# Kernel tuning notes

Hardware: AMD Instinct MI355X
Metric: run time of the kernel (lower is better)

The kernel has to match this reference:

```python
import jax, jax.numpy as jnp
from jax import lax
import numpy as np

P1, P2, M1, M2, WIN, STEP = 7, 7, 18, 55, 37, 4


def _unfold(x, p):
    # x: [N,C,Hp,Wp] -> [N, C*p*p, Ho*Wo], torch.nn.functional.unfold ordering (C, di, dj)
    N, C, Hp, Wp = x.shape
    Ho, Wo = Hp - p + 1, Wp - p + 1
    cols = jnp.stack([x[:, :, i:i + Ho, j:j + Wo] for i in range(p) for j in range(p)], axis=2)
    return cols.reshape(N, C * p * p, Ho * Wo)


def _reflect_unfold(x, r, p):
    return _unfold(jnp.pad(x, ((0, 0), (0, 0), (r, r), (r, r)), mode='reflect'), p)


def _fold(X, p, oh, ow):
    # inverse of unfold (sum of overlapping patches), torch.nn.functional.fold
    N, n, L = X.shape
    Ho, Wo = oh - p + 1, ow - p + 1
    C = n // (p * p)
    Xr = X.reshape(N, C, p, p, Ho, Wo)
    out = jnp.zeros((N, C, oh, ow), X.dtype)
    for i in range(p):
        for j in range(p):
            out = out.at[:, :, i:i + Ho, j:j + Wo].add(Xr[:, :, i, j])
    return out


def _block_matching(x, m, p, w, s):
    # x: [N,1,H,W] -> flat patch indices [N, B*m] into the (H+w-1)x(W+w-1) unfold grid
    N, C, H, Wd = x.shape
    inc = w // 2
    xs = _reflect_unfold(x, p // 2 + inc, p).reshape(N, p * p, H + 2 * inc, Wd + 2 * inc)
    xc = xs[:, :, inc:inc + H:s, inc:inc + Wd:s]  # [N, p*p, Hs, Ws]
    Hs, Ws = xc.shape[2], xc.shape[3]
    offs = jnp.stack(jnp.meshgrid(jnp.arange(w), jnp.arange(w), indexing='ij'), axis=-1).reshape(-1, 2)
    def d_of(off):
        xo = lax.dynamic_slice(xs, (0, 0, off[0], off[1]), (N, p * p, H, Wd))[:, :, ::s, ::s]
        return jnp.sum((xo - xc) ** 2, axis=1)  # [N, Hs, Ws]
    dist = jnp.moveaxis(lax.map(d_of, offs), 0, 1)  # [N, w*w, Hs, Ws]
    dist = dist.at[:, inc * w + inc].set(-1.0)  # force self-match first
    _, idx = lax.top_k(-jnp.transpose(dist, (0, 2, 3, 1)), m)  # smallest m, sorted
    idx = jnp.transpose(idx, (0, 3, 1, 2))  # [N, m, Hs, Ws]
    ir = idx // w - inc
    ic = idx % w - inc
    rows = inc + s * jnp.arange(Hs)
    cols = inc + s * jnp.arange(Ws)
    flat = (ir + rows[None, None, :, None]) * (Wd + w - 1) + (ic + cols[None, None, None, :])
    return jnp.transpose(flat.reshape(N, m, Hs * Ws), (0, 2, 1)).reshape(N, -1)  # [N, B*m]


def _group_patches(unf, idx, m, n):
    # unf: [N, n, L], idx: [N, B*m] -> [N, B, m, n]
    N = unf.shape[0]
    g = jnp.take_along_axis(unf, idx[:, None, :], axis=2)  # [N, n, B*m]
    return jnp.transpose(g, (0, 2, 1)).reshape(N, -1, m, n)


def _denoise1(Y, sigma):
    m, n = Y.shape[2], Y.shape[3]
    YtY = jnp.einsum('abik,abjk->abij', Y, Y)
    rhs = YtY - (n * sigma ** 2) * jnp.eye(m, dtype=Y.dtype)
    theta = jnp.swapaxes(jnp.linalg.solve(YtY, rhs), -1, -2)
    Xh = theta @ Y
    wts = 1.0 / jnp.sum(theta ** 2, axis=3, keepdims=True)
    return Xh, wts


def _denoise2(Y, X, sigma):
    m, n = X.shape[2], X.shape[3]
    XtX = jnp.einsum('abik,abjk->abij', X, X)
    A = XtX + (n * sigma ** 2) * jnp.eye(m, dtype=X.dtype)
    theta = jnp.swapaxes(jnp.linalg.solve(A, XtX), -1, -2)
    Xh = theta @ Y
    wts = 1.0 / jnp.sum(theta ** 2, axis=3, keepdims=True)
    return Xh, wts


def _aggregation(Y, wts, idx, H, Wd, L, p, w):
    # Y: [N,B,m,n], wts: [N,B,m,1], idx: [N,B*m]; scatter-add into unfold grid, fold, normalize
    N, B, m, n = Y.shape
    Yw = jnp.transpose(Y * wts, (0, 3, 1, 2)).reshape(N, n, B * m)
    wflat = jnp.broadcast_to(wts.reshape(N, 1, B * m), (N, n, B * m))
    def scat(vals, ib):
        return jnp.zeros((n, L), vals.dtype).at[:, ib].add(vals)
    Xsum = jax.vmap(scat)(Yw, idx)
    div = jax.vmap(scat)(wflat, idx)
    oh, ow = H + w - 1 + p - 1, Wd + w - 1 + p - 1
    num = _fold(Xsum, p, oh, ow)
    den = _fold(div, p, oh, ow)
    r = w // 2 + p // 2
    return (num / den)[:, :, r:-r, r:-r]


def _nlridge(input_y, sigma):
    N, C, H, Wd = input_y.shape
    w, s = WIN, STEP
    # ---- step 1 ----
    p, m = P1, M1
    yb = jnp.mean(input_y, axis=1, keepdims=True)
    idx1 = _block_matching(lax.stop_gradient(yb), m, p, w, s)
    unf_y1 = _reflect_unfold(input_y, p // 2 + w // 2, p)
    Y1 = _group_patches(unf_y1, idx1, m, C * p * p)
    Xh1, w1 = _denoise1(Y1, sigma)
    den1 = _aggregation(Xh1, w1, idx1, H, Wd, unf_y1.shape[2], p, w)
    # ---- step 2 ----
    p, m = P2, M2
    xb = jnp.mean(den1, axis=1, keepdims=True)
    idx2 = _block_matching(lax.stop_gradient(xb), m, p, w, s)
    unf_y2 = _reflect_unfold(input_y, p // 2 + w // 2, p)
    unf_x2 = _reflect_unfold(den1, p // 2 + w // 2, p)
    Y2 = _group_patches(unf_y2, idx2, m, C * p * p)
    X2 = _group_patches(unf_x2, idx2, m, C * p * p)
    Xh2, w2 = _denoise2(Y2, X2, sigma)
    return _aggregation(Xh2, w2, idx2, H, Wd, unf_y2.shape[2], p, w)


def setup_inputs() -> dict:
    key = jax.random.key(0)
    k1 = jax.random.fold_in(key, 1)
    input_y = jax.random.uniform(k1, (1, 1, 256, 256), dtype=jnp.float32)
    sigma = jnp.asarray(0.1, dtype=jnp.float32)  # ~25/255 AWGN
    return {"input_y": input_y, "sigma": sigma}


def reference(input_y, sigma):
    return _nlridge(input_y, sigma)
```

## Files before the change

### kernel.cpp

```cpp
#include <hip/hip_runtime.h>
#include <math.h>
#include <float.h>

constexpr int IMG  = 256;
constexpr int PADR = 21;
constexpr int PDIM = IMG + 2*PADR;
constexpr int XDIM = PDIM - 7 + 1;
constexpr int LTOT = XDIM * XDIM;
constexpr int WSZ  = 37;
constexpr int INC  = 18;
constexpr int ST   = 4;
constexpr int GDIM = 64;
constexpr int NBLK = GDIM * GDIM;
constexpr int PS   = 7;
constexpr int PP   = 49;
constexpr int MM1  = 18;
constexpr int MM2  = 55;
constexpr int RG   = 43;
constexpr int NOFF = WSZ * WSZ;
constexpr int UCAP = (NOFF + 63) / 64;

__global__ void pad_reflect(const float* __restrict__ src, float* __restrict__ dst)
{
    int idx = blockIdx.x * 256 + threadIdx.x;
    if (idx >= PDIM * PDIM) return;
    int y = idx / PDIM, x = idx % PDIM;
    int oy = y - PADR; oy = (oy < 0) ? -oy : ((oy >= IMG) ? 2*(IMG-1) - oy : oy);
    int ox = x - PADR; ox = (ox < 0) ? -ox : ((ox >= IMG) ? 2*(IMG-1) - ox : ox);
    dst[idx] = src[oy * IMG + ox];
}

__global__ __launch_bounds__(256) void block_match(const float* __restrict__ pad,
                                                   int* __restrict__ pos, int m)
{
    __shared__ float reg[RG][RG + 1];
    __shared__ float dist[NOFF];

    const int gi = blockIdx.y, gj = blockIdx.x;
    const int tid = threadIdx.x;
    const int r0 = ST * gi, c0 = ST * gj;

    for (int t = tid; t < RG * RG; t += 256) {
        int r = t / RG, c = t % RG;
        reg[r][c] = pad[(r0 + r) * PDIM + (c0 + c)];
    }
    __syncthreads();

    float q[PP];
#pragma unroll
    for (int i = 0; i < PS; i++)
#pragma unroll
        for (int j = 0; j < PS; j++)
            q[i * PS + j] = reg[INC + i][INC + j];

    for (int o = tid; o < NOFF; o += 256) {
        int oi = o / WSZ, oj = o % WSZ;
        float s = 0.f;
#pragma unroll
        for (int i = 0; i < PS; i++)
#pragma unroll
            for (int j = 0; j < PS; j++) {
                float d = reg[oi + i][oj + j] - q[i * PS + j];
                s += d * d;
            }
        dist[o] = (o == INC * WSZ + INC) ? -1.0f : s;
    }
    __syncthreads();

    if (tid >= 64) return;
    const int lane = tid;

    float dv[UCAP];
#pragma unroll
    for (int u = 0; u < UCAP; u++) {
        int o = lane + (u << 6);
        dv[u] = (o < NOFF) ? dist[o] : FLT_MAX;
    }

    const int blk = gi * GDIM + gj;
    for (int sel = 0; sel < m; sel++) {
        float bv = dv[0]; int bo = lane;
#pragma unroll
        for (int u = 1; u < UCAP; u++) {
            int o = lane + (u << 6);
            if (dv[u] < bv) { bv = dv[u]; bo = o; }
        }
#pragma unroll
        for (int d = 1; d < 64; d <<= 1) {
            float ov = __shfl_xor(bv, d);
            int   oo = __shfl_xor(bo, d);
            if (ov < bv || (ov == bv && oo < bo)) { bv = ov; bo = oo; }
        }
        if (lane == 0) {
            int oi = bo / WSZ, oj = bo % WSZ;
            pos[blk * m + sel] = (oi + ST * gi) * XDIM + (oj + ST * gj);
        }
#pragma unroll
        for (int u = 0; u < UCAP; u++)
            if (bo == lane + (u << 6)) dv[u] = FLT_MAX;
    }
}

template<int M_, bool ADDC>
__global__ __launch_bounds__(256) void denoise_scatter(
    const float* __restrict__ padY, const float* __restrict__ padS,
    const int* __restrict__ pos, const float* __restrict__ sigma_p,
    float* __restrict__ Num, float* __restrict__ Wacc)
{
    constexpr int MP = (M_ + 4) & ~3;
    constexpr int SS = 52;
    constexpr int YS = 60;

    __shared__ __align__(16) float Ssh[M_ * SS];
    __shared__ __align__(16) float Yt [PP * YS];
    __shared__ __align__(16) float Msh[M_ * MP];
    __shared__ float wsh[M_];
    __shared__ int   posh[M_];

    const int tid = threadIdx.x;
    const int blk = blockIdx.x;
    const float sg = *sigma_p;
    const float c  = (float)PP * sg * sg;

    if (tid < M_) posh[tid] = pos[blk * M_ + tid];
    __syncthreads();

    for (int t = tid; t < M_ * SS; t += 256) {
        int k = t / SS, qq = t - k * SS;
        float v = 0.f;
        if (qq < PP) {
            int p_ = posh[k];
            int a = p_ / XDIM, b = p_ - (p_ / XDIM) * XDIM;
            v = padS[(a + qq / PS) * PDIM + (b + qq % PS)];
        }
        Ssh[t] = v;
    }
    for (int t = tid; t < PP * M_; t += 256) {
        int qq = t / M_, k = t - qq * M_;
        int p_ = posh[k];
        int a = p_ / XDIM, b = p_ - (p_ / XDIM) * XDIM;
        Yt[qq * YS + k] = padY[(a + qq / PS) * PDIM + (b + qq % PS)];
    }
    __syncthreads();

    for (int t = tid; t < M_ * M_; t += 256) {
        int i = t / M_, j = t - i * M_;
        if (j > i) continue;
        const float4* Si = (const float4*)&Ssh[i * SS];
        const float4* Sj = (const float4*)&Ssh[j * SS];
        float acc = 0.f;
#pragma unroll
        for (int cch = 0; cch < SS / 4; cch++) {
            float4 a4 = Si[cch], b4 = Sj[cch];
            acc += a4.x * b4.x + a4.y * b4.y + a4.z * b4.z + a4.w * b4.w;
        }
        if (ADDC && i == j) acc += c;
        Msh[i * MP + j] = acc;
    }
    __syncthreads();

    if (tid < 64) {
        const int j = (tid < M_) ? tid : (M_ - 1);
        float col[M_];
#pragma unroll
        for (int i = 0; i < M_; i++)
            col[i] = Msh[(i >= j) ? (i * MP + j) : (j * MP + i)];

#pragma unroll
        for (int k = 0; k < M_; k++) {
            float d = __int_as_float(__builtin_amdgcn_readlane(__float_as_int(col[k]), k));
            d = (fabsf(d) > 1e-30f) ? d : 1e-30f;
            float dinv = 1.0f / d;
            float cks = col[k];
            float f  = (j == k) ? (1.0f - dinv) : (cks * dinv);
            float fn = -f;
#pragma unroll
            for (int i = 0; i < M_; i++) {
                if (i == k) continue;
                float aik = __int_as_float(__builtin_amdgcn_readlane(__float_as_int(cks), i));
                col[i] = fmaf(aik, fn, col[i]);
            }
            col[k] = (j == k) ? (-dinv) : (cks * dinv);
        }
        if (tid < M_) {
            float s = 0.f;
#pragma unroll
            for (int i = 0; i < M_; i++) {
                float th = fmaf(c, col[i], (i == j) ? 1.f : 0.f);
                s = fmaf(th, th, s);
            }
            wsh[j] = 1.0f / s;
#pragma unroll
            for (int i = 0; i < M_; i++)
                Msh[i * MP + j] = -col[i];
        }
    }
    __syncthreads();

    for (int t = tid; t < M_ * PP; t += 256) {
        int k = t / PP, qq = t - k * PP;
        const float4* Mi = (const float4*)&Msh[k * MP];
        const float4* Yq = (const float4*)&Yt [qq * YS];
        float z = 0.f;
#pragma unroll
        for (int cch = 0; cch < M_ / 4; cch++) {
            float4 a4 = Mi[cch], b4 = Yq[cch];
            z += a4.x * b4.x + a4.y * b4.y + a4.z * b4.z + a4.w * b4.w;
        }
#pragma unroll
        for (int jj = (M_ / 4) * 4; jj < M_; jj++)
            z += Msh[k * MP + jj] * Yt[qq * YS + jj];
        float xh = Yt[qq * YS + k] - c * z;
        int p_ = posh[k];
        int a = p_ / XDIM, b = p_ - (p_ / XDIM) * XDIM;
        atomicAdd(&Num[(a + qq / PS) * PDIM + (b + qq % PS)], xh * wsh[k]);
    }
    for (int t = tid; t < M_; t += 256)
        atomicAdd(&Wacc[posh[t]], wsh[t]);
}

__global__ void fold_norm(const float* __restrict__ Num, const float* __restrict__ Wacc,
                          float* __restrict__ out)
{
    int idx = blockIdx.x * 256 + threadIdx.x;
    if (idx >= IMG * IMG) return;
    int y0 = idx / IMG, x0 = idx % IMG;
    int y = y0 + PADR, x = x0 + PADR;
    float den = 0.f;
#pragma unroll
    for (int i = 0; i < PS; i++)
#pragma unroll
        for (int j = 0; j < PS; j++)
            den += Wacc[(y - i) * XDIM + (x - j)];
    out[idx] = Num[y * PDIM + x] / den;
}

extern "C" void kernel_launch(void* const* d_in, const int* in_sizes, int n_in,
                              void* d_out, int out_size, void* d_ws, size_t ws_size,
                              hipStream_t stream)
{
    const float* input = (const float*)d_in[0];
    const float* sigma = (const float*)d_in[1];
    float* out = (float*)d_out;

    char* ws = (char*)d_ws;
    float* padY = (float*)ws; ws += (size_t)PDIM * PDIM * 4;
    float* padX = (float*)ws; ws += (size_t)PDIM * PDIM * 4;
    float* den1 = (float*)ws; ws += (size_t)IMG * IMG * 4;
    int*   pos  = (int*)ws;   ws += (size_t)NBLK * MM2 * 4;
    float* Num  = (float*)ws; ws += (size_t)PDIM * PDIM * 4;
    float* Wacc = (float*)ws; ws += (size_t)LTOT * 4;

    const int padBlocks = (PDIM * PDIM + 255) / 256;
    const int imgBlocks = (IMG * IMG + 255) / 256;

    hipMemsetAsync(Num,  0, (size_t)PDIM * PDIM * 4, stream);
    hipMemsetAsync(Wacc, 0, (size_t)LTOT * 4, stream);
    pad_reflect<<<padBlocks, 256, 0, stream>>>(input, padY);
    block_match<<<dim3(GDIM, GDIM), 256, 0, stream>>>(padY, pos, MM1);
    denoise_scatter<MM1, false><<<NBLK, 256, 0, stream>>>(padY, padY, pos, sigma, Num, Wacc);
    fold_norm<<<imgBlocks, 256, 0, stream>>>(Num, Wacc, den1);

    pad_reflect<<<padBlocks, 256, 0, stream>>>(den1, padX);
    hipMemsetAsync(Num,  0, (size_t)PDIM * PDIM * 4, stream);
    hipMemsetAsync(Wacc, 0, (size_t)LTOT * 4, stream);
    block_match<<<dim3(GDIM, GDIM), 256, 0, stream>>>(padX, pos, MM2);
    denoise_scatter<MM2, true><<<NBLK, 256, 0, stream>>>(padY, padX, pos, sigma, Num, Wacc);
    fold_norm<<<imgBlocks, 256, 0, stream>>>(Num, Wacc, out);
}
```

Before: 1.086 ms.

## Scatter patch contributions per offset plane and fold in normalization

```diff
diff --git a/kernel.cpp b/kernel.cpp
--- a/kernel.cpp
+++ b/kernel.cpp
@@ -105,7 +105,7 @@
 __global__ __launch_bounds__(256) void denoise_scatter(
     const float* __restrict__ padY, const float* __restrict__ padS,
     const int* __restrict__ pos, const float* __restrict__ sigma_p,
-    float* __restrict__ Num, float* __restrict__ Wacc)
+    float* __restrict__ Xsum, float* __restrict__ Wacc)
 {
     constexpr int MP = (M_ + 4) & ~3;
     constexpr int SS = 52;
@@ -118,7 +118,7 @@
     __shared__ int   posh[M_];
 
     const int tid = threadIdx.x;
-    const int blk = blockIdx.x;
+    const int blk = (blockIdx.x * 1031) & (NBLK - 1);
     const float sg = *sigma_p;
     const float c  = (float)PP * sg * sg;
 
@@ -211,28 +211,29 @@
         for (int jj = (M_ / 4) * 4; jj < M_; jj++)
             z += Msh[k * MP + jj] * Yt[qq * YS + jj];
         float xh = Yt[qq * YS + k] - c * z;
-        int p_ = posh[k];
-        int a = p_ / XDIM, b = p_ - (p_ / XDIM) * XDIM;
-        atomicAdd(&Num[(a + qq / PS) * PDIM + (b + qq % PS)], xh * wsh[k]);
+        atomicAdd(&Xsum[qq * LTOT + posh[k]], xh * wsh[k]);
     }
     for (int t = tid; t < M_; t += 256)
         atomicAdd(&Wacc[posh[t]], wsh[t]);
 }
 
-__global__ void fold_norm(const float* __restrict__ Num, const float* __restrict__ Wacc,
+__global__ void fold_norm(const float* __restrict__ Xsum, const float* __restrict__ Wacc,
                           float* __restrict__ out)
 {
     int idx = blockIdx.x * 256 + threadIdx.x;
     if (idx >= IMG * IMG) return;
     int y0 = idx / IMG, x0 = idx % IMG;
     int y = y0 + PADR, x = x0 + PADR;
-    float den = 0.f;
+    float num = 0.f, den = 0.f;
 #pragma unroll
     for (int i = 0; i < PS; i++)
 #pragma unroll
-        for (int j = 0; j < PS; j++)
-            den += Wacc[(y - i) * XDIM + (x - j)];
-    out[idx] = Num[y * PDIM + x] / den;
+        for (int j = 0; j < PS; j++) {
+            int a = y - i, b = x - j;
+            num += Xsum[(i * PS + j) * LTOT + a * XDIM + b];
+            den += Wacc[a * XDIM + b];
+        }
+    out[idx] = num / den;
 }
 
 extern "C" void kernel_launch(void* const* d_in, const int* in_sizes, int n_in,
@@ -248,23 +249,23 @@
     float* padX = (float*)ws; ws += (size_t)PDIM * PDIM * 4;
     float* den1 = (float*)ws; ws += (size_t)IMG * IMG * 4;
     int*   pos  = (int*)ws;   ws += (size_t)NBLK * MM2 * 4;
-    float* Num  = (float*)ws; ws += (size_t)PDIM * PDIM * 4;
+    float* Xsum = (float*)ws; ws += (size_t)PP * LTOT * 4;
     float* Wacc = (float*)ws; ws += (size_t)LTOT * 4;
 
     const int padBlocks = (PDIM * PDIM + 255) / 256;
     const int imgBlocks = (IMG * IMG + 255) / 256;
 
-    hipMemsetAsync(Num,  0, (size_t)PDIM * PDIM * 4, stream);
+    hipMemsetAsync(Xsum, 0, (size_t)PP * LTOT * 4, stream);
     hipMemsetAsync(Wacc, 0, (size_t)LTOT * 4, stream);
     pad_reflect<<<padBlocks, 256, 0, stream>>>(input, padY);
     block_match<<<dim3(GDIM, GDIM), 256, 0, stream>>>(padY, pos, MM1);
-    denoise_scatter<MM1, false><<<NBLK, 256, 0, stream>>>(padY, padY, pos, sigma, Num, Wacc);
-    fold_norm<<<imgBlocks, 256, 0, stream>>>(Num, Wacc, den1);
+    denoise_scatter<MM1, false><<<NBLK, 256, 0, stream>>>(padY, padY, pos, sigma, Xsum, Wacc);
+    fold_norm<<<imgBlocks, 256, 0, stream>>>(Xsum, Wacc, den1);
 
     pad_reflect<<<padBlocks, 256, 0, stream>>>(den1, padX);
-    hipMemsetAsync(Num,  0, (size_t)PDIM * PDIM * 4, stream);
+    hipMemsetAsync(Xsum, 0, (size_t)PP * LTOT * 4, stream);
     hipMemsetAsync(Wacc, 0, (size_t)LTOT * 4, stream);
     block_match<<<dim3(GDIM, GDIM), 256, 0, stream>>>(padX, pos, MM2);
-    denoise_scatter<MM2, true><<<NBLK, 256, 0, stream>>>(padY, padX, pos, sigma, Num, Wacc);
-    fold_norm<<<imgBlocks, 256, 0, stream>>>(Num, Wacc, out);
-}
+    denoise_scatter<MM2, true><<<NBLK, 256, 0, stream>>>(padY, padX, pos, sigma, Xsum, Wacc);
+    fold_norm<<<imgBlocks, 256, 0, stream>>>(Xsum, Wacc, out);
+}
```

Measured after the change: 1.523 ms. +40.3%, slower.
